# Optimization experiments

Hardware: AMD Instinct MI355X
Metric: run time of the kernel (lower is better)

Reference implementation:

```python
import jax, jax.numpy as jnp
import numpy as np

N_NODES = 100000
N_EDGES = 3200000
D_NODE = 16
D_EDGE = 8
D_HIDDEN = 16


def setup_inputs() -> dict:
    key = jax.random.key(0)
    ks = jax.random.split(key, 8)
    node_features = jax.random.normal(ks[0], (N_NODES, D_NODE), dtype=jnp.float32)
    edge_attr_e3nn = jax.random.normal(ks[1], (N_EDGES, D_EDGE), dtype=jnp.float32)
    node_attr_scalar_raw = jax.random.normal(ks[2], (N_NODES, 1), dtype=jnp.float32)
    W_msg_tp = jax.random.normal(ks[3], (D_NODE, D_EDGE, D_HIDDEN), dtype=jnp.float32)
    W_msg_lin = jax.random.normal(ks[4], (D_HIDDEN, D_HIDDEN), dtype=jnp.float32)
    W_upd_tp = jax.random.normal(ks[5], (D_NODE, D_HIDDEN, D_HIDDEN), dtype=jnp.float32)
    W_upd_lin = jax.random.normal(ks[6], (D_HIDDEN, D_NODE), dtype=jnp.float32)
    edge_index = jax.random.randint(ks[7], (2, N_EDGES), 0, N_NODES, dtype=jnp.int64)
    return {
        "node_features": node_features,
        "edge_attr_e3nn": edge_attr_e3nn,
        "node_attr_scalar_raw": node_attr_scalar_raw,
        "W_msg_tp": W_msg_tp,
        "W_msg_lin": W_msg_lin,
        "W_upd_tp": W_upd_tp,
        "W_upd_lin": W_upd_lin,
        "edge_index": edge_index,
    }


def reference(node_features, edge_attr_e3nn, node_attr_scalar_raw,
              W_msg_tp, W_msg_lin, W_upd_tp, W_upd_lin, edge_index):
    n_nodes = node_features.shape[0]
    row = edge_index[0]  # destination (aggregation target)
    col = edge_index[1]  # source (gathered neighbor)

    # fan-in normalizations (e3nn FullyConnectedTensorProduct / Linear convention)
    norm_msg_tp = 1.0 / np.float32(np.sqrt(D_NODE * D_EDGE))
    norm_upd_tp = 1.0 / np.float32(np.sqrt(D_NODE * D_HIDDEN))
    norm_lin = 1.0 / np.float32(np.sqrt(D_HIDDEN))

    # --- message step: gather -> bilinear TP -> gate -> linear ---
    x_j = node_features[col]                                   # [E, D_node]
    m = jnp.einsum('ei,ej,ijh->eh', x_j, edge_attr_e3nn, W_msg_tp) * norm_msg_tp
    m = jax.nn.silu(m)                                         # gate nonlinearity
    m = (m @ W_msg_lin) * norm_lin                             # [E, D_hidden]

    # --- scatter-sum aggregation into nodes ---
    agg = jax.ops.segment_sum(m, row, num_segments=n_nodes)    # [N, D_hidden]

    # --- update step: bilinear TP -> gate -> linear -> residual ---
    u = jnp.einsum('ni,nh,ihk->nk', node_features, agg, W_upd_tp) * norm_upd_tp
    u = jax.nn.silu(u)
    u = (u @ W_upd_lin) * norm_lin                             # [N, D_node]

    return node_features + u
```

## Files before the change

### kernel.cpp

```cpp
#include <hip/hip_runtime.h>
#include <math.h>

#define N_NODES_C 100000
#define N_EDGES_C 3200000

#define NORM_MSG_TP 0.08838834764831845f
#define NORM_UPD_TP 0.0625f
#define NORM_LIN    0.25f

typedef float f32x4 __attribute__((ext_vector_type(4)));
typedef short bf16x8 __attribute__((ext_vector_type(8)));
typedef int   int4v  __attribute__((ext_vector_type(4)));

__device__ __forceinline__ float silu_f(float v) {
  return v / (1.0f + __expf(-v));
}

__device__ __forceinline__ void atomic_add_hw(float* p, float v) {
  unsafeAtomicAdd(p, v);
}

__device__ __forceinline__ unsigned int bf16_bits(float f) {
  unsigned int b = __float_as_uint(f);
  return (b + 0x7fffu + ((b >> 16) & 1u)) >> 16;
}
__device__ __forceinline__ unsigned int pack_bf16x2(float lo, float hi) {
  return bf16_bits(lo) | (bf16_bits(hi) << 16);
}
__device__ __forceinline__ float unlo(unsigned int w) { return __uint_as_float(w << 16); }
__device__ __forceinline__ float unhi(unsigned int w) { return __uint_as_float(w & 0xffff0000u); }


__global__ __launch_bounds__(256) void zero_ints(int* __restrict__ p, int n) {
  int i = blockIdx.x * 256 + threadIdx.x;
  if (i < n) p[i] = 0;
}

__global__ __launch_bounds__(256) void hist_kernel(
    const int* __restrict__ row, int* __restrict__ cnt, int* __restrict__ pos) {
  int e = blockIdx.x * 256 + threadIdx.x;
  pos[e] = atomicAdd(&cnt[row[e]], 1);
}

__global__ __launch_bounds__(256) void scan_block(
    const int* __restrict__ cnt, int* __restrict__ off, int* __restrict__ bsum, int n) {
  __shared__ int s[256];
  const int t = threadIdx.x;
  const int i = blockIdx.x * 256 + t;
  const int v = (i < n) ? cnt[i] : 0;
  s[t] = v;
  __syncthreads();
#pragma unroll
  for (int o = 1; o < 256; o <<= 1) {
    int tv = (t >= o) ? s[t - o] : 0;
    __syncthreads();
    s[t] += tv;
    __syncthreads();
  }
  if (i < n) off[i] = s[t] - v;
  if (t == 255) bsum[blockIdx.x] = s[255];
}

__global__ void scan_bsum(int* __restrict__ bsum, int nb) {
  __shared__ int s[512];
  const int t = threadIdx.x;
  const int v = (t < nb) ? bsum[t] : 0;
  s[t] = v;
  __syncthreads();
#pragma unroll
  for (int o = 1; o < 512; o <<= 1) {
    int tv = (t >= o) ? s[t - o] : 0;
    __syncthreads();
    s[t] += tv;
    __syncthreads();
  }
  if (t < nb) bsum[t] = s[t] - v;
}

__global__ __launch_bounds__(256) void scan_add(
    int* __restrict__ off, const int* __restrict__ bsum, int n, int total) {
  int i = blockIdx.x * 256 + threadIdx.x;
  if (i < n) off[i] += bsum[blockIdx.x];
  if (i == 0) off[n] = total;
}


__global__ __launch_bounds__(256) void xcast_kernel(
    const float* __restrict__ x, unsigned short* __restrict__ xb) {
  const int i = blockIdx.x * 256 + threadIdx.x;
  if (i < N_NODES_C * 2) {
    const float4 a = *reinterpret_cast<const float4*>(x + (size_t)i * 8);
    const float4 b = *reinterpret_cast<const float4*>(x + (size_t)i * 8 + 4);
    uint4 w;
    w.x = pack_bf16x2(a.x, a.y); w.y = pack_bf16x2(a.z, a.w);
    w.z = pack_bf16x2(b.x, b.y); w.w = pack_bf16x2(b.z, b.w);
    *reinterpret_cast<uint4*>(xb + (size_t)i * 8) = w;
  }
}


#define CLAIM_TILE(T, CC, PP) do {                                   \
    const int e_ = (T) * 16 + el;                                    \
    CC = __builtin_nontemporal_load(&eidx[N_EDGES_C + e_]);          \
    const int rd_ = __builtin_nontemporal_load(&eidx[e_]);           \
    PP = off[rd_] + __builtin_nontemporal_load(&pos[e_]);            \
  } while (0)

#define GATH_TILE(T, CC, XH, FA, FB) do {                            \
    const int e_ = (T) * 16 + el;                                    \
    XH = *reinterpret_cast<const uint4*>(xb + (size_t)(CC) * 16 + 8 * ghalf); \
    FA = __builtin_nontemporal_load(                                 \
        reinterpret_cast<const f32x4*>(ea + (size_t)e_ * 8));        \
    FB = __builtin_nontemporal_load(                                 \
        reinterpret_cast<const f32x4*>(ea + (size_t)e_ * 8 + 4));    \
  } while (0)

__global__ __launch_bounds__(256) void place5_kernel(
    const int*   __restrict__ eidx,
    const float* __restrict__ ea,
    const float* __restrict__ Wtp,
    const int*   __restrict__ off,
    const int*   __restrict__ pos,
    const unsigned short* __restrict__ xb,
    unsigned int* __restrict__ msort)
{
  const int lane  = threadIdx.x & 63;
  const int el    = lane & 15;
  const int g     = lane >> 4;
  const int gsel  = g >> 1;
  const int ghalf = g & 1;

  bf16x8 aq[4];
#pragma unroll
  for (int q = 0; q < 4; ++q) {
#pragma unroll
    for (int t = 0; t < 8; ++t) {
      const float w = Wtp[(8 * ghalf + t) * 128 + (2 * q + gsel) * 16 + el];
      aq[q][t] = (short)bf16_bits(w);
    }
  }

  const int s = gridDim.x * 4;
  const int wid = blockIdx.x * 4 + (threadIdx.x >> 6);
  const int ntiles = N_EDGES_C / 16;

  int cc_a = 0, pp_a = 0, cc_b = 0, pp_b = 0;
  uint4 xh_a; xh_a.x = xh_a.y = xh_a.z = xh_a.w = 0;
  f32x4 fa_a = {0.f, 0.f, 0.f, 0.f}, fb_a = {0.f, 0.f, 0.f, 0.f};

  if (wid < ntiles)     CLAIM_TILE(wid, cc_a, pp_a);
  if (wid + s < ntiles) CLAIM_TILE(wid + s, cc_b, pp_b);
  if (wid < ntiles)     GATH_TILE(wid, cc_a, xh_a, fa_a, fb_a);

  for (int t = wid; t < ntiles; t += s) {
    int cc_c = 0, pp_c = 0;
    if (t + 2 * s < ntiles) CLAIM_TILE(t + 2 * s, cc_c, pp_c);
    uint4 xh_b; xh_b.x = xh_b.y = xh_b.z = xh_b.w = 0;
    f32x4 fa_b = {0.f, 0.f, 0.f, 0.f}, fb_b = {0.f, 0.f, 0.f, 0.f};
    if (t + s < ntiles) GATH_TILE(t + s, cc_b, xh_b, fa_b, fb_b);

    float xf[8];
    xf[0] = unlo(xh_a.x); xf[1] = unhi(xh_a.x);
    xf[2] = unlo(xh_a.y); xf[3] = unhi(xh_a.y);
    xf[4] = unlo(xh_a.z); xf[5] = unhi(xh_a.z);
    xf[6] = unlo(xh_a.w); xf[7] = unhi(xh_a.w);
    float eq[4];
    eq[0] = gsel ? fa_a[1] : fa_a[0];
    eq[1] = gsel ? fa_a[3] : fa_a[2];
    eq[2] = gsel ? fb_a[1] : fb_a[0];
    eq[3] = gsel ? fb_a[3] : fb_a[2];

    f32x4 acc = {0.f, 0.f, 0.f, 0.f};
#pragma unroll
    for (int q = 0; q < 4; ++q) {
      const float e_ = eq[q];
      const unsigned u0 = __float_as_uint(xf[0] * e_) + 0x8000u;
      const unsigned u1 = __float_as_uint(xf[1] * e_) + 0x8000u;
      const unsigned u2 = __float_as_uint(xf[2] * e_) + 0x8000u;
      const unsigned u3 = __float_as_uint(xf[3] * e_) + 0x8000u;
      const unsigned u4 = __float_as_uint(xf[4] * e_) + 0x8000u;
      const unsigned u5 = __float_as_uint(xf[5] * e_) + 0x8000u;
      const unsigned u6 = __float_as_uint(xf[6] * e_) + 0x8000u;
      const unsigned u7 = __float_as_uint(xf[7] * e_) + 0x8000u;
      int4v iv;
      iv.x = (int)__builtin_amdgcn_perm(u1, u0, 0x07060302u);
      iv.y = (int)__builtin_amdgcn_perm(u3, u2, 0x07060302u);
      iv.z = (int)__builtin_amdgcn_perm(u5, u4, 0x07060302u);
      iv.w = (int)__builtin_amdgcn_perm(u7, u6, 0x07060302u);
      union { int4v i; bf16x8 h; } cv; cv.i = iv;
      acc = __builtin_amdgcn_mfma_f32_16x16x32_bf16(aq[q], cv.h, acc, 0, 0, 0);
    }

    const float o0 = silu_f(acc[0] * NORM_MSG_TP);
    const float o1 = silu_f(acc[1] * NORM_MSG_TP);
    const float o2 = silu_f(acc[2] * NORM_MSG_TP);
    const float o3 = silu_f(acc[3] * NORM_MSG_TP);
    const unsigned long long wout =
        (unsigned long long)pack_bf16x2(o0, o1) |
        ((unsigned long long)pack_bf16x2(o2, o3) << 32);
    __builtin_nontemporal_store(
        wout, reinterpret_cast<unsigned long long*>(&msort[(size_t)pp_a * 8 + g * 2]));

    cc_a = cc_b; pp_a = pp_b; xh_a = xh_b; fa_a = fa_b; fb_a = fb_b;
    cc_b = cc_c; pp_b = pp_c;
  }
}


__global__ __launch_bounds__(256) void agg3_kernel(
    const float* __restrict__ Wlin,
    const unsigned int* __restrict__ msort,
    const int*   __restrict__ off,
    float*       __restrict__ agg)
{
  __shared__ float sL[256];
  if (threadIdx.x < 256) sL[threadIdx.x] = Wlin[threadIdx.x];
  __syncthreads();

  const int slane = threadIdx.x & 15;
  const int n = blockIdx.x * 16 + (threadIdx.x >> 4);

  const int off0 = off[n];
  const int off1 = off[n + 1];

  float acc = 0.f;
  for (int p = off0; p < off1; ++p) {
    const unsigned int w = msort[(size_t)p * 8 + (slane >> 1)];
    acc += (slane & 1) ? unhi(w) : unlo(w);
  }

  float a = 0.f;
#pragma unroll
  for (int h = 0; h < 16; ++h) {
    const float v = __shfl(acc, h, 16);
    a = fmaf(v, sL[h * 16 + slane], a);
  }
  agg[(size_t)n * 16 + slane] = a * NORM_LIN;
}


__global__ __launch_bounds__(256) void tbuild_kernel(
    const float* __restrict__ x, const float* __restrict__ Wtp,
    uint4* __restrict__ Tb)
{
  __shared__ float sWT[16 * 132];
  for (int idx = threadIdx.x; idx < 2048; idx += 256) {
    const int i = idx >> 7, j = (idx >> 4) & 7, h = idx & 15;
    sWT[h * 132 + i * 8 + j] = Wtp[idx];
  }
  __syncthreads();

  const int slane = threadIdx.x & 15;
  const int n = blockIdx.x * 16 + (threadIdx.x >> 4);

  float xr[16];
  const float4* xp = reinterpret_cast<const float4*>(x + (size_t)n * 16);
#pragma unroll
  for (int q = 0; q < 4; ++q) {
    float4 v = xp[q];
    xr[q*4+0] = v.x; xr[q*4+1] = v.y; xr[q*4+2] = v.z; xr[q*4+3] = v.w;
  }

  float t[8];
#pragma unroll
  for (int j = 0; j < 8; ++j) t[j] = 0.f;
#pragma unroll
  for (int i = 0; i < 16; ++i) {
    const float xi = xr[i];
    const float4 wa = *reinterpret_cast<const float4*>(&sWT[slane * 132 + i * 8]);
    const float4 wb = *reinterpret_cast<const float4*>(&sWT[slane * 132 + i * 8 + 4]);
    t[0] = fmaf(xi, wa.x, t[0]); t[1] = fmaf(xi, wa.y, t[1]);
    t[2] = fmaf(xi, wa.z, t[2]); t[3] = fmaf(xi, wa.w, t[3]);
    t[4] = fmaf(xi, wb.x, t[4]); t[5] = fmaf(xi, wb.y, t[5]);
    t[6] = fmaf(xi, wb.z, t[6]); t[7] = fmaf(xi, wb.w, t[7]);
  }
  uint4 w;
  w.x = pack_bf16x2(t[0], t[1]);
  w.y = pack_bf16x2(t[2], t[3]);
  w.z = pack_bf16x2(t[4], t[5]);
  w.w = pack_bf16x2(t[6], t[7]);
  Tb[(size_t)n * 16 + slane] = w;
}

__global__ __launch_bounds__(256) void place_kernel(
    const int* __restrict__ eidx, const float* __restrict__ ea,
    const int* __restrict__ off, int* __restrict__ cnt,
    int* __restrict__ colp, uint4* __restrict__ eab) {
  int e = blockIdx.x * 256 + threadIdx.x;
  const int r = eidx[e];
  const int old = atomicSub(&cnt[r], 1);
  const int p = off[r] + old - 1;
  colp[p] = eidx[N_EDGES_C + e];
  const float4* ep = reinterpret_cast<const float4*>(ea + (size_t)e * 8);
  const float4 a = ep[0];
  const float4 b = ep[1];
  uint4 w;
  w.x = pack_bf16x2(a.x, a.y);
  w.y = pack_bf16x2(a.z, a.w);
  w.z = pack_bf16x2(b.x, b.y);
  w.w = pack_bf16x2(b.z, b.w);
  eab[p] = w;
}

__global__ __launch_bounds__(256) void agg2_kernel(
    const float* __restrict__ Wlin, const int* __restrict__ colp,
    const uint4* __restrict__ eab, const uint4* __restrict__ Tb,
    const int* __restrict__ off, float* __restrict__ agg)
{
  __shared__ float sL[256];
  if (threadIdx.x < 256) sL[threadIdx.x] = Wlin[threadIdx.x];
  __syncthreads();

  const int slane = threadIdx.x & 15;
  const int n = blockIdx.x * 16 + (threadIdx.x >> 4);

  const int off0 = off[n];
  const int off1 = off[n + 1];

  float acc = 0.f;
#pragma unroll 2
  for (int p = off0; p < off1; ++p) {
    const int c = colp[p];
    const uint4 tw = Tb[(size_t)c * 16 + slane];
    const uint4 ew = eab[p];
    float m;
    m  = unlo(ew.x) * unlo(tw.x);
    m  = fmaf(unhi(ew.x), unhi(tw.x), m);
    m  = fmaf(unlo(ew.y), unlo(tw.y), m);
    m  = fmaf(unhi(ew.y), unhi(tw.y), m);
    m  = fmaf(unlo(ew.z), unlo(tw.z), m);
    m  = fmaf(unhi(ew.z), unhi(tw.z), m);
    m  = fmaf(unlo(ew.w), unlo(tw.w), m);
    m  = fmaf(unhi(ew.w), unhi(tw.w), m);
    acc += silu_f(m * NORM_MSG_TP);
  }

  float a = 0.f;
#pragma unroll
  for (int h = 0; h < 16; ++h) {
    const float v = __shfl(acc, h, 16);
    a = fmaf(v, sL[h * 16 + slane], a);
  }
  agg[(size_t)n * 16 + slane] = a * NORM_LIN;
}


__global__ __launch_bounds__(256) void node_kernel(
    const float* __restrict__ x, const float* __restrict__ agg,
    const float* __restrict__ Wtp, const float* __restrict__ Wlin,
    float* __restrict__ out)
{
  __shared__ float sW[4096];
  __shared__ float sL[256];
  for (int t = threadIdx.x; t < 4096; t += 256) sW[t] = Wtp[t];
  sL[threadIdx.x] = Wlin[threadIdx.x];
  __syncthreads();

  const long n = (long)blockIdx.x * 256 + threadIdx.x;
  if (n >= N_NODES_C) return;

  float xr[16], ar[16];
  const float4* xp = reinterpret_cast<const float4*>(x + (size_t)n * 16);
  const float4* ap = reinterpret_cast<const float4*>(agg + (size_t)n * 16);
#pragma unroll
  for (int q = 0; q < 4; ++q) {
    float4 v = xp[q];
    xr[q*4+0] = v.x; xr[q*4+1] = v.y; xr[q*4+2] = v.z; xr[q*4+3] = v.w;
    float4 w = ap[q];
    ar[q*4+0] = w.x; ar[q*4+1] = w.y; ar[q*4+2] = w.z; ar[q*4+3] = w.w;
  }
  float u[16];
#pragma unroll
  for (int k = 0; k < 16; ++k) u[k] = 0.f;
#pragma unroll
  for (int i = 0; i < 16; ++i) {
#pragma unroll
    for (int h = 0; h < 16; ++h) {
      const float p = xr[i] * ar[h];
      const float* w = &sW[(i*16 + h) * 16];
#pragma unroll
      for (int k = 0; k < 16; ++k) u[k] = fmaf(p, w[k], u[k]);
    }
  }
  float g[16];
#pragma unroll
  for (int k = 0; k < 16; ++k) g[k] = silu_f(u[k] * NORM_UPD_TP);
  float res[16];
#pragma unroll
  for (int k2 = 0; k2 < 16; ++k2) {
    float a = 0.f;
#pragma unroll
    for (int k = 0; k < 16; ++k) a = fmaf(g[k], sL[k*16 + k2], a);
    res[k2] = xr[k2] + a * NORM_LIN;
  }
  float4* op = reinterpret_cast<float4*>(out + (size_t)n * 16);
#pragma unroll
  for (int q = 0; q < 4; ++q)
    op[q] = make_float4(res[q*4+0], res[q*4+1], res[q*4+2], res[q*4+3]);
}


__global__ void zero_f4(float4* __restrict__ p, int n4) {
  int i = blockIdx.x * blockDim.x + threadIdx.x;
  if (i < n4) p[i] = make_float4(0.f, 0.f, 0.f, 0.f);
}

#define EPT 2
__global__ __launch_bounds__(256) void edge_kernel(
    const float* __restrict__ x, const float* __restrict__ ea,
    const float* __restrict__ Wtp, const float* __restrict__ Wlin,
    const int* __restrict__ eidx, float* __restrict__ agg)
{
  __shared__ float sW[2048];
  __shared__ float sL[256];
  for (int t = threadIdx.x; t < 2048; t += 256) sW[t] = Wtp[t];
  sL[threadIdx.x] = Wlin[threadIdx.x];
  __syncthreads();
  const long e0 = ((long)blockIdx.x * 256 + threadIdx.x) * EPT;
  float xr[EPT][16], er[EPT][8];
  int rw[EPT];
#pragma unroll
  for (int e = 0; e < EPT; ++e) {
    const long ei = e0 + e;
    const int c = eidx[N_EDGES_C + ei];
    rw[e] = eidx[ei];
    const float4* xp = reinterpret_cast<const float4*>(x + (size_t)c * 16);
#pragma unroll
    for (int q = 0; q < 4; ++q) {
      float4 v = xp[q];
      xr[e][q*4+0] = v.x; xr[e][q*4+1] = v.y; xr[e][q*4+2] = v.z; xr[e][q*4+3] = v.w;
    }
    const float4* ep = reinterpret_cast<const float4*>(ea + (size_t)ei * 8);
#pragma unroll
    for (int q = 0; q < 2; ++q) {
      float4 v = ep[q];
      er[e][q*4+0] = v.x; er[e][q*4+1] = v.y; er[e][q*4+2] = v.z; er[e][q*4+3] = v.w;
    }
  }
  float m[EPT][16];
#pragma unroll
  for (int e = 0; e < EPT; ++e)
#pragma unroll
    for (int h = 0; h < 16; ++h) m[e][h] = 0.f;
#pragma unroll
  for (int i = 0; i < 16; ++i) {
#pragma unroll
    for (int j = 0; j < 8; ++j) {
      float p[EPT];
#pragma unroll
      for (int e = 0; e < EPT; ++e) p[e] = xr[e][i] * er[e][j];
      const float* w = &sW[(i*8 + j) * 16];
#pragma unroll
      for (int h = 0; h < 16; ++h) {
        const float wv = w[h];
#pragma unroll
        for (int e = 0; e < EPT; ++e) m[e][h] = fmaf(p[e], wv, m[e][h]);
      }
    }
  }
#pragma unroll
  for (int e = 0; e < EPT; ++e) {
    float g[16];
#pragma unroll
    for (int h = 0; h < 16; ++h) g[h] = silu_f(m[e][h] * NORM_MSG_TP);
    float* ap = agg + (size_t)rw[e] * 16;
#pragma unroll
    for (int h2 = 0; h2 < 16; ++h2) {
      float a = 0.f;
#pragma unroll
      for (int h = 0; h < 16; ++h) a = fmaf(g[h], sL[h*16 + h2], a);
      atomic_add_hw(ap + h2, a * NORM_LIN);
    }
  }
}


extern "C" void kernel_launch(void* const* d_in, const int* in_sizes, int n_in,
                              void* d_out, int out_size, void* d_ws, size_t ws_size,
                              hipStream_t stream) {
  const float* node_features = (const float*)d_in[0];
  const float* edge_attr     = (const float*)d_in[1];
  const float* W_msg_tp      = (const float*)d_in[3];
  const float* W_msg_lin     = (const float*)d_in[4];
  const float* W_upd_tp      = (const float*)d_in[5];
  const float* W_upd_lin     = (const float*)d_in[6];
  const int*   edge_index    = (const int*)d_in[7];
  float* out = (float*)d_out;
  char* ws = (char*)d_ws;

  const int NB_N = (N_NODES_C + 255) / 256;
  const int NB_E = N_EDGES_C / 256;
  const int NB_G = N_NODES_C / 16;

  const size_t A_OFF  = 0;
  const size_t A_CNT  = 400128;
  const size_t A_BSUM = 800256;
  const size_t A_POS  = 802304;
  const size_t A_MSORT= A_POS + 12800000;
  const size_t A_XB   = A_MSORT + 102400000;
  const size_t A_NEED = A_XB + 3200000;

  const size_t B_OFF  = 0;
  const size_t B_CNT  = 400128;
  const size_t B_BSUM = 800256;
  const size_t B_COLP = 804352;
  const size_t B_EAB  = B_COLP + 12800000;
  const size_t B_T    = B_EAB + 51200000;
  const size_t B_AGG  = B_T + 25600000;
  const size_t B_NEED = B_AGG + 6400000;

  if (ws_size >= A_NEED) {
    int*   off   = (int*)(ws + A_OFF);
    int*   cnt   = (int*)(ws + A_CNT);
    int*   bsum  = (int*)(ws + A_BSUM);
    int*   pos   = (int*)(ws + A_POS);
    unsigned int* msort = (unsigned int*)(ws + A_MSORT);
    unsigned short* xb  = (unsigned short*)(ws + A_XB);
    float* agg   = (float*)(ws + A_POS);

    hipLaunchKernelGGL(zero_ints, dim3(NB_N), dim3(256), 0, stream, cnt, N_NODES_C);
    hipLaunchKernelGGL(hist_kernel, dim3(NB_E), dim3(256), 0, stream,
                       edge_index, cnt, pos);
    hipLaunchKernelGGL(scan_block, dim3(NB_N), dim3(256), 0, stream,
                       cnt, off, bsum, N_NODES_C);
    hipLaunchKernelGGL(scan_bsum, dim3(1), dim3(512), 0, stream, bsum, NB_N);
    hipLaunchKernelGGL(scan_add, dim3(NB_N), dim3(256), 0, stream,
                       off, bsum, N_NODES_C, N_EDGES_C);
    hipLaunchKernelGGL(xcast_kernel, dim3((N_NODES_C * 2 + 255) / 256), dim3(256),
                       0, stream, node_features, xb);
    hipLaunchKernelGGL(place5_kernel, dim3(2048), dim3(256), 0, stream,
                       edge_index, edge_attr, W_msg_tp, off, pos, xb, msort);
    hipLaunchKernelGGL(agg3_kernel, dim3(NB_G), dim3(256), 0, stream,
                       W_msg_lin, msort, off, agg);
    hipLaunchKernelGGL(node_kernel, dim3(NB_N), dim3(256), 0, stream,
                       node_features, agg, W_upd_tp, W_upd_lin, out);
  } else if (ws_size >= B_NEED) {
    int*   off  = (int*)(ws + B_OFF);
    int*   cnt  = (int*)(ws + B_CNT);
    int*   bsum = (int*)(ws + B_BSUM);
    int*   colp = (int*)(ws + B_COLP);
    uint4* eab  = (uint4*)(ws + B_EAB);
    uint4* Tb   = (uint4*)(ws + B_T);
    float* agg  = (float*)(ws + B_AGG);

    hipLaunchKernelGGL(zero_ints, dim3(NB_N), dim3(256), 0, stream, cnt, N_NODES_C);
    hipLaunchKernelGGL(hist_kernel, dim3(NB_E), dim3(256), 0, stream,
                       edge_index, cnt, colp );
    hipLaunchKernelGGL(scan_block, dim3(NB_N), dim3(256), 0, stream,
                       cnt, off, bsum, N_NODES_C);
    hipLaunchKernelGGL(scan_bsum, dim3(1), dim3(512), 0, stream, bsum, NB_N);
    hipLaunchKernelGGL(scan_add, dim3(NB_N), dim3(256), 0, stream,
                       off, bsum, N_NODES_C, N_EDGES_C);
    hipLaunchKernelGGL(place_kernel, dim3(NB_E), dim3(256), 0, stream,
                       edge_index, edge_attr, off, cnt, colp, eab);
    hipLaunchKernelGGL(tbuild_kernel, dim3(NB_G), dim3(256), 0, stream,
                       node_features, W_msg_tp, Tb);
    hipLaunchKernelGGL(agg2_kernel, dim3(NB_G), dim3(256), 0, stream,
                       W_msg_lin, colp, eab, Tb, off, agg);
    hipLaunchKernelGGL(node_kernel, dim3(NB_N), dim3(256), 0, stream,
                       node_features, agg, W_upd_tp, W_upd_lin, out);
  } else {
    float* agg = (float*)ws;
    const int n4 = N_NODES_C * 16 / 4;
    hipLaunchKernelGGL(zero_f4, dim3((n4 + 255) / 256), dim3(256), 0, stream,
                       (float4*)agg, n4);
    hipLaunchKernelGGL(edge_kernel, dim3(N_EDGES_C / (256 * EPT)), dim3(256), 0, stream,
                       node_features, edge_attr, W_msg_tp, W_msg_lin, edge_index, agg);
    hipLaunchKernelGGL(node_kernel, dim3(NB_N), dim3(256), 0, stream,
                       node_features, agg, W_upd_tp, W_upd_lin, out);
  }
}
```

Baseline: 426.9 us.

## Replace global counting sort with per-block bucketized edge lists and LDS aggregation

Drops the global histogram, three-pass scan and scattered message placement. A single bucketize kernel now groups edge ids into 128-node buckets per 8000-edge chunk, messages are written in plain edge order, and a bucket-aggregation kernel gathers each bucket's messages and accumulates them with LDS atomics before applying the linear layer. This trades global atomics and random message writes for random message reads plus shared-memory atomics, and the bagg kernel now walks 400 chunk segments per bucket.

```diff
diff --git a/kernel.cpp b/kernel.cpp
--- a/kernel.cpp
+++ b/kernel.cpp
@@ -8,6 +8,11 @@
 #define NORM_UPD_TP 0.0625f
 #define NORM_LIN    0.25f
 
+#define NBUK  782
+#define NBUKP 784
+#define BPB   8000
+#define NBLK_BUK 400
+
 typedef float f32x4 __attribute__((ext_vector_type(4)));
 typedef short bf16x8 __attribute__((ext_vector_type(8)));
 typedef int   int4v  __attribute__((ext_vector_type(4)));
@@ -31,57 +36,64 @@
 __device__ __forceinline__ float unhi(unsigned int w) { return __uint_as_float(w & 0xffff0000u); }
 
 
-__global__ __launch_bounds__(256) void zero_ints(int* __restrict__ p, int n) {
-  int i = blockIdx.x * 256 + threadIdx.x;
-  if (i < n) p[i] = 0;
-}
-
-__global__ __launch_bounds__(256) void hist_kernel(
-    const int* __restrict__ row, int* __restrict__ cnt, int* __restrict__ pos) {
-  int e = blockIdx.x * 256 + threadIdx.x;
-  pos[e] = atomicAdd(&cnt[row[e]], 1);
-}
-
-__global__ __launch_bounds__(256) void scan_block(
-    const int* __restrict__ cnt, int* __restrict__ off, int* __restrict__ bsum, int n) {
-  __shared__ int s[256];
+__global__ __launch_bounds__(256) void bucketize_kernel(
+    const int* __restrict__ row,
+    int* __restrict__ bids,
+    int* __restrict__ sct)
+{
+  __shared__ int lhist[NBUKP];
+  __shared__ int lcur[NBUKP];
+  __shared__ int partial[256];
+  __shared__ int lids[BPB];
   const int t = threadIdx.x;
-  const int i = blockIdx.x * 256 + t;
-  const int v = (i < n) ? cnt[i] : 0;
-  s[t] = v;
-  __syncthreads();
-#pragma unroll
+  const int base = blockIdx.x * BPB;
+
+  for (int i = t; i < NBUKP; i += 256) lhist[i] = 0;
+  __syncthreads();
+  for (int k = t; k < BPB; k += 256)
+    atomicAdd(&lhist[row[base + k] >> 7], 1);
+  __syncthreads();
+
+  int csum = 0;
+  if (t < 196) {
+    int s = 0;
+#pragma unroll
+    for (int j = 0; j < 4; ++j) {
+      const int v = lhist[t * 4 + j];
+      lhist[t * 4 + j] = s;
+      s += v;
+    }
+    csum = s;
+  }
+  partial[t] = csum;
+  __syncthreads();
   for (int o = 1; o < 256; o <<= 1) {
-    int tv = (t >= o) ? s[t - o] : 0;
+    int tv = (t >= o) ? partial[t - o] : 0;
     __syncthreads();
-    s[t] += tv;
+    partial[t] += tv;
     __syncthreads();
   }
-  if (i < n) off[i] = s[t] - v;
-  if (t == 255) bsum[blockIdx.x] = s[255];
-}
-
-__global__ void scan_bsum(int* __restrict__ bsum, int nb) {
-  __shared__ int s[512];
-  const int t = threadIdx.x;
-  const int v = (t < nb) ? bsum[t] : 0;
-  s[t] = v;
-  __syncthreads();
-#pragma unroll
-  for (int o = 1; o < 512; o <<= 1) {
-    int tv = (t >= o) ? s[t - o] : 0;
-    __syncthreads();
-    s[t] += tv;
-    __syncthreads();
-  }
-  if (t < nb) bsum[t] = s[t] - v;
-}
-
-__global__ __launch_bounds__(256) void scan_add(
-    int* __restrict__ off, const int* __restrict__ bsum, int n, int total) {
-  int i = blockIdx.x * 256 + threadIdx.x;
-  if (i < n) off[i] += bsum[blockIdx.x];
-  if (i == 0) off[n] = total;
+  const int add = partial[t] - csum;
+  if (t < 196) {
+#pragma unroll
+    for (int j = 0; j < 4; ++j) lhist[t * 4 + j] += add;
+  }
+  __syncthreads();
+  for (int i = t; i < NBUKP; i += 256) lcur[i] = lhist[i];
+  __syncthreads();
+
+  for (int k = t; k < BPB; k += 256) {
+    const int r = row[base + k];
+    const int b = r >> 7;
+    const int p = atomicAdd(&lcur[b], 1);
+    lids[p] = ((base + k) << 7) | (r & 127);
+  }
+  __syncthreads();
+
+  for (int i = t; i < NBUKP; i += 256)
+    sct[blockIdx.x * NBUKP + i] = lhist[i];
+  for (int k = t; k < BPB; k += 256)
+    bids[base + k] = lids[k];
 }
 
 
@@ -99,11 +111,8 @@
 }
 
 
-#define CLAIM_TILE(T, CC, PP) do {                                   \
-    const int e_ = (T) * 16 + el;                                    \
-    CC = __builtin_nontemporal_load(&eidx[N_EDGES_C + e_]);          \
-    const int rd_ = __builtin_nontemporal_load(&eidx[e_]);           \
-    PP = off[rd_] + __builtin_nontemporal_load(&pos[e_]);            \
+#define COLS_TILE(T, CC) do {                                        \
+    CC = __builtin_nontemporal_load(&eidx[N_EDGES_C + (T) * 16 + el]); \
   } while (0)
 
 #define GATH_TILE(T, CC, XH, FA, FB) do {                            \
@@ -115,14 +124,12 @@
         reinterpret_cast<const f32x4*>(ea + (size_t)e_ * 8 + 4));    \
   } while (0)
 
-__global__ __launch_bounds__(256) void place5_kernel(
+__global__ __launch_bounds__(256) void msg6_kernel(
     const int*   __restrict__ eidx,
     const float* __restrict__ ea,
     const float* __restrict__ Wtp,
-    const int*   __restrict__ off,
-    const int*   __restrict__ pos,
     const unsigned short* __restrict__ xb,
-    unsigned int* __restrict__ msort)
+    unsigned int* __restrict__ msgb)
 {
   const int lane  = threadIdx.x & 63;
   const int el    = lane & 15;
@@ -144,17 +151,17 @@
   const int wid = blockIdx.x * 4 + (threadIdx.x >> 6);
   const int ntiles = N_EDGES_C / 16;
 
-  int cc_a = 0, pp_a = 0, cc_b = 0, pp_b = 0;
+  int cc_a = 0, cc_b = 0;
   uint4 xh_a; xh_a.x = xh_a.y = xh_a.z = xh_a.w = 0;
   f32x4 fa_a = {0.f, 0.f, 0.f, 0.f}, fb_a = {0.f, 0.f, 0.f, 0.f};
 
-  if (wid < ntiles)     CLAIM_TILE(wid, cc_a, pp_a);
-  if (wid + s < ntiles) CLAIM_TILE(wid + s, cc_b, pp_b);
+  if (wid < ntiles)     COLS_TILE(wid, cc_a);
+  if (wid + s < ntiles) COLS_TILE(wid + s, cc_b);
   if (wid < ntiles)     GATH_TILE(wid, cc_a, xh_a, fa_a, fb_a);
 
   for (int t = wid; t < ntiles; t += s) {
-    int cc_c = 0, pp_c = 0;
-    if (t + 2 * s < ntiles) CLAIM_TILE(t + 2 * s, cc_c, pp_c);
+    int cc_c = 0;
+    if (t + 2 * s < ntiles) COLS_TILE(t + 2 * s, cc_c);
     uint4 xh_b; xh_b.x = xh_b.y = xh_b.z = xh_b.w = 0;
     f32x4 fa_b = {0.f, 0.f, 0.f, 0.f}, fb_b = {0.f, 0.f, 0.f, 0.f};
     if (t + s < ntiles) GATH_TILE(t + s, cc_b, xh_b, fa_b, fb_b);
@@ -199,45 +206,169 @@
         (unsigned long long)pack_bf16x2(o0, o1) |
         ((unsigned long long)pack_bf16x2(o2, o3) << 32);
     __builtin_nontemporal_store(
-        wout, reinterpret_cast<unsigned long long*>(&msort[(size_t)pp_a * 8 + g * 2]));
-
-    cc_a = cc_b; pp_a = pp_b; xh_a = xh_b; fa_a = fa_b; fb_a = fb_b;
-    cc_b = cc_c; pp_b = pp_c;
-  }
-}
-
-
-__global__ __launch_bounds__(256) void agg3_kernel(
+        wout, reinterpret_cast<unsigned long long*>(
+                  &msgb[(size_t)(t * 16 + el) * 8 + g * 2]));
+
+    cc_a = cc_b; xh_a = xh_b; fa_a = fa_b; fb_a = fb_b;
+    cc_b = cc_c;
+  }
+}
+
+
+__global__ __launch_bounds__(256) void bagg_kernel(
+    const int* __restrict__ sct,
+    const int* __restrict__ bids,
+    const unsigned int* __restrict__ msgb,
     const float* __restrict__ Wlin,
-    const unsigned int* __restrict__ msort,
-    const int*   __restrict__ off,
-    float*       __restrict__ agg)
+    float* __restrict__ agg)
 {
+  __shared__ float lagg[128][16];
   __shared__ float sL[256];
-  if (threadIdx.x < 256) sL[threadIdx.x] = Wlin[threadIdx.x];
-  __syncthreads();
-
-  const int slane = threadIdx.x & 15;
-  const int n = blockIdx.x * 16 + (threadIdx.x >> 4);
-
-  const int off0 = off[n];
-  const int off1 = off[n + 1];
-
-  float acc = 0.f;
-  for (int p = off0; p < off1; ++p) {
-    const unsigned int w = msort[(size_t)p * 8 + (slane >> 1)];
-    acc += (slane & 1) ? unhi(w) : unlo(w);
-  }
-
-  float a = 0.f;
-#pragma unroll
-  for (int h = 0; h < 16; ++h) {
-    const float v = __shfl(acc, h, 16);
-    a = fmaf(v, sL[h * 16 + slane], a);
-  }
-  agg[(size_t)n * 16 + slane] = a * NORM_LIN;
-}
-
+  const int t = threadIdx.x;
+  const int b = blockIdx.x;
+  sL[t] = Wlin[t];
+  for (int i = t; i < 2048; i += 256) (&lagg[0][0])[i] = 0.f;
+  __syncthreads();
+
+  const int slane = t & 15;
+  const int grp   = t >> 4;
+
+  for (int blk = grp; blk < NBLK_BUK; blk += 16) {
+    const int s = sct[blk * NBUKP + b];
+    const int e = sct[blk * NBUKP + b + 1];
+    for (int k = s; k < e; ++k) {
+      const int code  = bids[blk * BPB + k];
+      const int eid   = code >> 7;
+      const int local = code & 127;
+      const unsigned w = msgb[(size_t)eid * 8 + (slane >> 1)];
+      const float v = (slane & 1) ? unhi(w) : unlo(w);
+      atomicAdd(&lagg[local][slane], v);
+    }
+  }
+  __syncthreads();
+
+#pragma unroll
+  for (int i = 0; i < 8; ++i) {
+    const int idx = t * 8 + i;
+    const int node = idx >> 4, k2 = idx & 15;
+    const int n = b * 128 + node;
+    if (n < N_NODES_C) {
+      float a = 0.f;
+#pragma unroll
+      for (int h = 0; h < 16; ++h) a = fmaf(lagg[node][h], sL[h * 16 + k2], a);
+      agg[(size_t)n * 16 + k2] = a * NORM_LIN;
+    }
+  }
+}
+
+
+__global__ __launch_bounds__(256) void node_kernel(
+    const float* __restrict__ x, const float* __restrict__ agg,
+    const float* __restrict__ Wtp, const float* __restrict__ Wlin,
+    float* __restrict__ out)
+{
+  __shared__ float sW[4096];
+  __shared__ float sL[256];
+  for (int t = threadIdx.x; t < 4096; t += 256) sW[t] = Wtp[t];
+  sL[threadIdx.x] = Wlin[threadIdx.x];
+  __syncthreads();
+
+  const long n = (long)blockIdx.x * 256 + threadIdx.x;
+  if (n >= N_NODES_C) return;
+
+  float xr[16], ar[16];
+  const float4* xp = reinterpret_cast<const float4*>(x + (size_t)n * 16);
+  const float4* ap = reinterpret_cast<const float4*>(agg + (size_t)n * 16);
+#pragma unroll
+  for (int q = 0; q < 4; ++q) {
+    float4 v = xp[q];
+    xr[q*4+0] = v.x; xr[q*4+1] = v.y; xr[q*4+2] = v.z; xr[q*4+3] = v.w;
+    float4 w = ap[q];
+    ar[q*4+0] = w.x; ar[q*4+1] = w.y; ar[q*4+2] = w.z; ar[q*4+3] = w.w;
+  }
+  float u[16];
+#pragma unroll
+  for (int k = 0; k < 16; ++k) u[k] = 0.f;
+#pragma unroll
+  for (int i = 0; i < 16; ++i) {
+#pragma unroll
+    for (int h = 0; h < 16; ++h) {
+      const float p = xr[i] * ar[h];
+      const float* w = &sW[(i*16 + h) * 16];
+#pragma unroll
+      for (int k = 0; k < 16; ++k) u[k] = fmaf(p, w[k], u[k]);
+    }
+  }
+  float g[16];
+#pragma unroll
+  for (int k = 0; k < 16; ++k) g[k] = silu_f(u[k] * NORM_UPD_TP);
+  float res[16];
+#pragma unroll
+  for (int k2 = 0; k2 < 16; ++k2) {
+    float a = 0.f;
+#pragma unroll
+    for (int k = 0; k < 16; ++k) a = fmaf(g[k], sL[k*16 + k2], a);
+    res[k2] = xr[k2] + a * NORM_LIN;
+  }
+  float4* op = reinterpret_cast<float4*>(out + (size_t)n * 16);
+#pragma unroll
+  for (int q = 0; q < 4; ++q)
+    op[q] = make_float4(res[q*4+0], res[q*4+1], res[q*4+2], res[q*4+3]);
+}
+
+
+__global__ __launch_bounds__(256) void zero_ints(int* __restrict__ p, int n) {
+  int i = blockIdx.x * 256 + threadIdx.x;
+  if (i < n) p[i] = 0;
+}
+
+__global__ __launch_bounds__(256) void hist_kernel(
+    const int* __restrict__ row, int* __restrict__ cnt, int* __restrict__ pos) {
+  int e = blockIdx.x * 256 + threadIdx.x;
+  pos[e] = atomicAdd(&cnt[row[e]], 1);
+}
+
+__global__ __launch_bounds__(256) void scan_block(
+    const int* __restrict__ cnt, int* __restrict__ off, int* __restrict__ bsum, int n) {
+  __shared__ int s[256];
+  const int t = threadIdx.x;
+  const int i = blockIdx.x * 256 + t;
+  const int v = (i < n) ? cnt[i] : 0;
+  s[t] = v;
+  __syncthreads();
+#pragma unroll
+  for (int o = 1; o < 256; o <<= 1) {
+    int tv = (t >= o) ? s[t - o] : 0;
+    __syncthreads();
+    s[t] += tv;
+    __syncthreads();
+  }
+  if (i < n) off[i] = s[t] - v;
+  if (t == 255) bsum[blockIdx.x] = s[255];
+}
+
+__global__ void scan_bsum(int* __restrict__ bsum, int nb) {
+  __shared__ int s[512];
+  const int t = threadIdx.x;
+  const int v = (t < nb) ? bsum[t] : 0;
+  s[t] = v;
+  __syncthreads();
+#pragma unroll
+  for (int o = 1; o < 512; o <<= 1) {
+    int tv = (t >= o) ? s[t - o] : 0;
+    __syncthreads();
+    s[t] += tv;
+    __syncthreads();
+  }
+  if (t < nb) bsum[t] = s[t] - v;
+}
+
+__global__ __launch_bounds__(256) void scan_add(
+    int* __restrict__ off, const int* __restrict__ bsum, int n, int total) {
+  int i = blockIdx.x * 256 + threadIdx.x;
+  if (i < n) off[i] += bsum[blockIdx.x];
+  if (i == 0) off[n] = total;
+}
 
 __global__ __launch_bounds__(256) void tbuild_kernel(
     const float* __restrict__ x, const float* __restrict__ Wtp,
@@ -345,61 +476,6 @@
 }
 
 
-__global__ __launch_bounds__(256) void node_kernel(
-    const float* __restrict__ x, const float* __restrict__ agg,
-    const float* __restrict__ Wtp, const float* __restrict__ Wlin,
-    float* __restrict__ out)
-{
-  __shared__ float sW[4096];
-  __shared__ float sL[256];
-  for (int t = threadIdx.x; t < 4096; t += 256) sW[t] = Wtp[t];
-  sL[threadIdx.x] = Wlin[threadIdx.x];
-  __syncthreads();
-
-  const long n = (long)blockIdx.x * 256 + threadIdx.x;
-  if (n >= N_NODES_C) return;
-
-  float xr[16], ar[16];
-  const float4* xp = reinterpret_cast<const float4*>(x + (size_t)n * 16);
-  const float4* ap = reinterpret_cast<const float4*>(agg + (size_t)n * 16);
-#pragma unroll
-  for (int q = 0; q < 4; ++q) {
-    float4 v = xp[q];
-    xr[q*4+0] = v.x; xr[q*4+1] = v.y; xr[q*4+2] = v.z; xr[q*4+3] = v.w;
-    float4 w = ap[q];
-    ar[q*4+0] = w.x; ar[q*4+1] = w.y; ar[q*4+2] = w.z; ar[q*4+3] = w.w;
-  }
-  float u[16];
-#pragma unroll
-  for (int k = 0; k < 16; ++k) u[k] = 0.f;
-#pragma unroll
-  for (int i = 0; i < 16; ++i) {
-#pragma unroll
-    for (int h = 0; h < 16; ++h) {
-      const float p = xr[i] * ar[h];
-      const float* w = &sW[(i*16 + h) * 16];
-#pragma unroll
-      for (int k = 0; k < 16; ++k) u[k] = fmaf(p, w[k], u[k]);
-    }
-  }
-  float g[16];
-#pragma unroll
-  for (int k = 0; k < 16; ++k) g[k] = silu_f(u[k] * NORM_UPD_TP);
-  float res[16];
-#pragma unroll
-  for (int k2 = 0; k2 < 16; ++k2) {
-    float a = 0.f;
-#pragma unroll
-    for (int k = 0; k < 16; ++k) a = fmaf(g[k], sL[k*16 + k2], a);
-    res[k2] = xr[k2] + a * NORM_LIN;
-  }
-  float4* op = reinterpret_cast<float4*>(out + (size_t)n * 16);
-#pragma unroll
-  for (int q = 0; q < 4; ++q)
-    op[q] = make_float4(res[q*4+0], res[q*4+1], res[q*4+2], res[q*4+3]);
-}
-
-
 __global__ void zero_f4(float4* __restrict__ p, int n4) {
   int i = blockIdx.x * blockDim.x + threadIdx.x;
   if (i < n4) p[i] = make_float4(0.f, 0.f, 0.f, 0.f);
@@ -492,13 +568,12 @@
   const int NB_E = N_EDGES_C / 256;
   const int NB_G = N_NODES_C / 16;
 
-  const size_t A_OFF  = 0;
-  const size_t A_CNT  = 400128;
-  const size_t A_BSUM = 800256;
-  const size_t A_POS  = 802304;
-  const size_t A_MSORT= A_POS + 12800000;
-  const size_t A_XB   = A_MSORT + 102400000;
-  const size_t A_NEED = A_XB + 3200000;
+  const size_t A_SCT  = 0;
+  const size_t A_BIDS = 1254400;
+  const size_t A_MSGB = A_BIDS + 12800000;
+  const size_t A_XB   = A_MSGB + 102400000;
+  const size_t A_AGG  = A_XB + 3200000;
+  const size_t A_NEED = A_AGG + 6400000;
 
   const size_t B_OFF  = 0;
   const size_t B_CNT  = 400128;
@@ -510,28 +585,20 @@
   const size_t B_NEED = B_AGG + 6400000;
 
   if (ws_size >= A_NEED) {
-    int*   off   = (int*)(ws + A_OFF);
-    int*   cnt   = (int*)(ws + A_CNT);
-    int*   bsum  = (int*)(ws + A_BSUM);
-    int*   pos   = (int*)(ws + A_POS);
-    unsigned int* msort = (unsigned int*)(ws + A_MSORT);
-    unsigned short* xb  = (unsigned short*)(ws + A_XB);
-    float* agg   = (float*)(ws + A_POS);
-
-    hipLaunchKernelGGL(zero_ints, dim3(NB_N), dim3(256), 0, stream, cnt, N_NODES_C);
-    hipLaunchKernelGGL(hist_kernel, dim3(NB_E), dim3(256), 0, stream,
-                       edge_index, cnt, pos);
-    hipLaunchKernelGGL(scan_block, dim3(NB_N), dim3(256), 0, stream,
-                       cnt, off, bsum, N_NODES_C);
-    hipLaunchKernelGGL(scan_bsum, dim3(1), dim3(512), 0, stream, bsum, NB_N);
-    hipLaunchKernelGGL(scan_add, dim3(NB_N), dim3(256), 0, stream,
-                       off, bsum, N_NODES_C, N_EDGES_C);
+    int* sct   = (int*)(ws + A_SCT);
+    int* bids  = (int*)(ws + A_BIDS);
+    unsigned int* msgb = (unsigned int*)(ws + A_MSGB);
+    unsigned short* xb = (unsigned short*)(ws + A_XB);
+    float* agg = (float*)(ws + A_AGG);
+
+    hipLaunchKernelGGL(bucketize_kernel, dim3(NBLK_BUK), dim3(256), 0, stream,
+                       edge_index, bids, sct);
     hipLaunchKernelGGL(xcast_kernel, dim3((N_NODES_C * 2 + 255) / 256), dim3(256),
                        0, stream, node_features, xb);
-    hipLaunchKernelGGL(place5_kernel, dim3(2048), dim3(256), 0, stream,
-                       edge_index, edge_attr, W_msg_tp, off, pos, xb, msort);
-    hipLaunchKernelGGL(agg3_kernel, dim3(NB_G), dim3(256), 0, stream,
-                       W_msg_lin, msort, off, agg);
+    hipLaunchKernelGGL(msg6_kernel, dim3(2048), dim3(256), 0, stream,
+                       edge_index, edge_attr, W_msg_tp, xb, msgb);
+    hipLaunchKernelGGL(bagg_kernel, dim3(NBUK), dim3(256), 0, stream,
+                       sct, bids, msgb, W_msg_lin, agg);
     hipLaunchKernelGGL(node_kernel, dim3(NB_N), dim3(256), 0, stream,
                        node_features, agg, W_upd_tp, W_upd_lin, out);
   } else if (ws_size >= B_NEED) {
```

After: 540.5 us. 1.27x slower.
